# Kernel tuning notes

Measured on AMD Instinct MI355X. Metric: run time of the kernel, lower is better.

## Reference

```python
import jax, jax.numpy as jnp
import numpy as np

B, N, C, H = 4, 2048, 1024, 16
D = C // H  # head_dim = 64

def setup_inputs() -> dict:
    key = jax.random.key(0)
    k1, k2, k3, k4, k5, k6 = jax.random.split(key, 6)
    x = jax.random.normal(k1, (B, N, C), dtype=jnp.float32)
    rope_cos = jax.random.uniform(k2, (N, D), dtype=jnp.float32)
    rope_sin = jax.random.uniform(k3, (N, D), dtype=jnp.float32)
    w_qkv = jax.random.normal(k4, (3 * C, C), dtype=jnp.float32) * (C ** -0.5)
    w_proj = jax.random.normal(k5, (C, C), dtype=jnp.float32) * (C ** -0.5)
    b_proj = jax.random.normal(k6, (C,), dtype=jnp.float32) * 0.01
    return {"x": x, "rope_cos": rope_cos, "rope_sin": rope_sin,
            "w_qkv": w_qkv, "w_proj": w_proj, "b_proj": b_proj}

def _rotate_half(x):
    x1, x2 = jnp.split(x, 2, axis=-1)
    return jnp.concatenate((-x2, x1), axis=-1)

def _apply_rope(x, cos, sin):
    # x: [B,H,N,D]; cos/sin: [N,D] broadcast over B,H
    return x * cos + _rotate_half(x) * sin

def reference(x, rope_cos, rope_sin, w_qkv, w_proj, b_proj):
    Bc, Nc, Cc = x.shape
    scale = D ** -0.5
    qkv = jnp.einsum('bnc,fc->bnf', x, w_qkv)            # [B,N,3C]
    qkv = qkv.reshape(Bc, Nc, 3, H, D).transpose(2, 0, 3, 1, 4)  # [3,B,H,N,D]
    q, k, v = qkv[0], qkv[1], qkv[2]
    q = _apply_rope(q, rope_cos, rope_sin)
    k = _apply_rope(k, rope_cos, rope_sin)
    attn = jnp.einsum('bhnd,bhmd->bhnm', q, k) * scale   # [B,H,N,N]
    attn = jax.nn.softmax(attn, axis=-1)
    out = jnp.einsum('bhnm,bhmd->bhnd', attn, v)         # [B,H,N,D]
    out = out.transpose(0, 2, 1, 3).reshape(Bc, Nc, Cc)  # [B,N,C]
    return jnp.einsum('bnc,fc->bnf', out, w_proj) + b_proj
```

## Files before the change

kernel.cpp:

```cpp
#include <hip/hip_runtime.h>

#define MM   8192
#define CC   1024
#define F3   3072
#define NN   2048
#define HH   16
#define DD   64
#define QSCALE 0.1803368801111731f

typedef __attribute__((ext_vector_type(8))) __bf16 bf16x8;
typedef __attribute__((ext_vector_type(4))) float floatx4;
typedef __attribute__((ext_vector_type(4))) unsigned uintx4;

__device__ __forceinline__ unsigned short f2b(float f) {
  union { float f; unsigned int u; } v; v.f = f;
  unsigned int r = v.u + 0x7fffu + ((v.u >> 16) & 1u);
  return (unsigned short)(r >> 16);
}
__device__ __forceinline__ float b2f(unsigned short b) {
  union { unsigned int u; float f; } v; v.u = ((unsigned int)b) << 16;
  return v.f;
}

__device__ __forceinline__ void gl_lds16(const unsigned short* g, unsigned short* l) {
  __builtin_amdgcn_global_load_lds((const __attribute__((address_space(1))) void*)g,
                                   (__attribute__((address_space(3))) void*)l, 16, 0, 0);
}

__global__ __launch_bounds__(256) void f32_to_bf16_k(const float* __restrict__ in,
                                                     unsigned short* __restrict__ out, int n4) {
  int i = blockIdx.x * 256 + threadIdx.x;
  if (i < n4) {
    float4 v = ((const float4*)in)[i];
    ushort4 o;
    o.x = f2b(v.x); o.y = f2b(v.y); o.z = f2b(v.z); o.w = f2b(v.w);
    ((ushort4*)out)[i] = o;
  }
}

template <int F, bool BF16OUT, bool ROPE>
__global__ __launch_bounds__(256) void gemm_bt(const unsigned short* __restrict__ A,
                                               const unsigned short* __restrict__ Bm,
                                               void* __restrict__ Cout,
                                               const float* __restrict__ bias,
                                               const float* __restrict__ rcp,
                                               const float* __restrict__ spp, int K) {
  __shared__ alignas(16) unsigned short lA[128 * 32];
  __shared__ alignas(16) unsigned short lB[128 * 32];
  const int tid = threadIdx.x, lane = tid & 63, wave = tid >> 6;
  const int r16 = lane & 15, q4 = lane >> 4;
  const int rowBase = blockIdx.x * 128, colBase = blockIdx.y * 128;
  const int wm = wave & 1, wf = wave >> 1;

  floatx4 acc[4][4];
  const floatx4 z = {0.f, 0.f, 0.f, 0.f};
  for (int i = 0; i < 4; ++i)
    for (int j = 0; j < 4; ++j) acc[i][j] = z;

  for (int k0 = 0; k0 < K; k0 += 32) {
    __syncthreads();
#pragma unroll
    for (int i = 0; i < 2; ++i) {
      int chunk = i * 256 + tid;
      int row = chunk >> 2, col = (chunk & 3) * 8;
      gl_lds16(A + (size_t)(rowBase + row) * K + k0 + col, &lA[chunk * 8]);
      gl_lds16(Bm + (size_t)(colBase + row) * K + k0 + col, &lB[chunk * 8]);
    }
    __syncthreads();
    bf16x8 af[4];
    for (int im = 0; im < 4; ++im)
      af[im] = *(const bf16x8*)(&lA[(wm * 64 + im * 16 + r16) * 32 + q4 * 8]);
    for (int jf = 0; jf < 4; ++jf) {
      bf16x8 bfr = *(const bf16x8*)(&lB[(wf * 64 + jf * 16 + r16) * 32 + q4 * 8]);
      for (int im = 0; im < 4; ++im)
        acc[im][jf] = __builtin_amdgcn_mfma_f32_16x16x32_bf16(af[im], bfr, acc[im][jf], 0, 0, 0);
    }
  }

  if (ROPE) {
    int head = (colBase >> 6) + wf;
    if (head < 32) {
      const bool isq = head < 16;
      for (int im = 0; im < 4; ++im)
        for (int jf = 0; jf < 2; ++jf)
          for (int r = 0; r < 4; ++r) {
            int grow = rowBase + wm * 64 + im * 16 + q4 * 4 + r;
            int n = grow & (NN - 1);
            int dp = jf * 16 + r16;
            float x0 = acc[im][jf][r], x1 = acc[im][jf + 2][r];
            float c0 = rcp[n * DD + dp],      s0v = spp[n * DD + dp];
            float c1 = rcp[n * DD + dp + 32], s1v = spp[n * DD + dp + 32];
            float y0 = x0 * c0 - x1 * s0v;
            float y1 = x1 * c1 + x0 * s1v;
            if (isq) { y0 *= QSCALE; y1 *= QSCALE; }
            acc[im][jf][r] = y0;
            acc[im][jf + 2][r] = y1;
          }
    }
  }

  for (int im = 0; im < 4; ++im)
    for (int jf = 0; jf < 4; ++jf)
      for (int r = 0; r < 4; ++r) {
        int grow = rowBase + wm * 64 + im * 16 + q4 * 4 + r;
        int gcol = colBase + wf * 64 + jf * 16 + r16;
        if (BF16OUT)
          ((unsigned short*)Cout)[(size_t)grow * F + gcol] = f2b(acc[im][jf][r]);
        else
          ((float*)Cout)[(size_t)grow * F + gcol] = acc[im][jf][r] + bias[gcol];
      }
}

__global__ __launch_bounds__(256, 4) void attn_k(const unsigned short* __restrict__ qkv,
                                                 unsigned short* __restrict__ obuf) {
  __shared__ alignas(16) unsigned short sK[64 * 64];
  __shared__ alignas(16) unsigned short sVT[64 * 64];

  const int tid = threadIdx.x, lane = tid & 63, wave = tid >> 6;
  const int r16 = lane & 15, q4 = lane >> 4;

  const int id = blockIdx.x + (int)gridDim.x * blockIdx.y;
  const int xcd = id & 7, slot = id >> 3;
  const int bh = xcd * 8 + (slot >> 4);
  const int q0 = (slot & 15) * 128;
  const int b = bh >> 4, h = bh & 15;
  const unsigned short* qbase = qkv + (size_t)(b * NN) * F3 + h * DD;

  bf16x8 qf[2][2];
#pragma unroll
  for (int im = 0; im < 2; ++im)
#pragma unroll
    for (int kk = 0; kk < 2; ++kk)
      qf[im][kk] = *(const bf16x8*)(qbase +
          (size_t)(q0 + wave * 32 + im * 16 + r16) * F3 + kk * 32 + q4 * 8);

  const floatx4 z = {0.f, 0.f, 0.f, 0.f};
  floatx4 o[2][4];
  float lacc[2] = {0.f, 0.f};
#pragma unroll
  for (int im = 0; im < 2; ++im)
    for (int jd = 0; jd < 4; ++jd) o[im][jd] = z;

  const int krow0 = tid >> 3, kc8 = tid & 7;
  const int vkvp = tid >> 3, vc8 = tid & 7;
  const int mp = (vkvp & 16) | ((vkvp & 4) << 1) | ((vkvp & 2) << 1) |
                 ((vkvp & 8) >> 2) | (vkvp & 1);

  const unsigned short* kvb = qbase;
  int4 kreg0 = *(const int4*)(kvb + (size_t)krow0 * F3 + CC + kc8 * 8);
  int4 kreg1 = *(const int4*)(kvb + (size_t)(krow0 + 32) * F3 + CC + kc8 * 8);
  int4 vreg0 = *(const int4*)(kvb + (size_t)(2 * vkvp) * F3 + 2 * CC + vc8 * 8);
  int4 vreg1 = *(const int4*)(kvb + (size_t)(2 * vkvp + 1) * F3 + 2 * CC + vc8 * 8);

  for (int t = 0; t < NN / 64; ++t) {
    __syncthreads();

    *(int4*)(&sK[krow0 * 64 + ((kc8 ^ (krow0 & 7)) << 3)]) = kreg0;
    *(int4*)(&sK[(krow0 + 32) * 64 + ((kc8 ^ ((krow0 + 32) & 7)) << 3)]) = kreg1;
    {
      const unsigned* a0 = (const unsigned*)&vreg0;
      const unsigned* a1 = (const unsigned*)&vreg1;
#pragma unroll
      for (int w = 0; w < 4; ++w) {
        unsigned lo = __builtin_amdgcn_perm(a1[w], a0[w], 0x05040100u);
        unsigned hi = __builtin_amdgcn_perm(a1[w], a0[w], 0x07060302u);
        int d0 = vc8 * 8 + 2 * w;
        int sw0 = (2 * w + vc8) & 7;
        int sw1 = (2 * w + 1 + vc8) & 7;
        *(unsigned*)(&sVT[d0 * 64 + (((mp >> 2) ^ sw0) << 3) + 2 * (mp & 3)]) = lo;
        *(unsigned*)(&sVT[(d0 + 1) * 64 + (((mp >> 2) ^ sw1) << 3) + 2 * (mp & 3)]) = hi;
      }
    }

    if (t + 1 < NN / 64) {
      const unsigned short* nb = qkv + (size_t)(b * NN + (t + 1) * 64) * F3 + h * DD;
      kreg0 = *(const int4*)(nb + (size_t)krow0 * F3 + CC + kc8 * 8);
      kreg1 = *(const int4*)(nb + (size_t)(krow0 + 32) * F3 + CC + kc8 * 8);
      vreg0 = *(const int4*)(nb + (size_t)(2 * vkvp) * F3 + 2 * CC + vc8 * 8);
      vreg1 = *(const int4*)(nb + (size_t)(2 * vkvp + 1) * F3 + 2 * CC + vc8 * 8);
    }

    __syncthreads();

    floatx4 s[2][4];
    __builtin_amdgcn_s_setprio(1);
#pragma unroll
    for (int jn = 0; jn < 4; ++jn) {
      int row = jn * 16 + r16;
      bf16x8 kf0 = *(const bf16x8*)(&sK[row * 64 + ((q4 ^ (row & 7)) << 3)]);
      bf16x8 kf1 = *(const bf16x8*)(&sK[row * 64 + (((4 + q4) ^ (row & 7)) << 3)]);
#pragma unroll
      for (int im = 0; im < 2; ++im) {
        floatx4 a = z;
        a = __builtin_amdgcn_mfma_f32_16x16x32_bf16(kf0, qf[im][0], a, 0, 0, 0);
        a = __builtin_amdgcn_mfma_f32_16x16x32_bf16(kf1, qf[im][1], a, 0, 0, 0);
        s[im][jn] = a;
      }
    }
    __builtin_amdgcn_s_setprio(0);

    bf16x8 pf[2][2];
#pragma unroll
    for (int im = 0; im < 2; ++im) {
#pragma unroll
      for (int kk = 0; kk < 2; ++kk) {
        uintx4 pk;
#pragma unroll
        for (int j2 = 0; j2 < 2; ++j2) {
          int jn = 2 * kk + j2;
          float p0 = __builtin_amdgcn_exp2f(s[im][jn][0]);
          float p1 = __builtin_amdgcn_exp2f(s[im][jn][1]);
          float p2 = __builtin_amdgcn_exp2f(s[im][jn][2]);
          float p3 = __builtin_amdgcn_exp2f(s[im][jn][3]);
          lacc[im] += (p0 + p1) + (p2 + p3);
          asm("v_cvt_pk_bf16_f32 %0, %1, %2" : "=v"(pk[2 * j2]) : "v"(p0), "v"(p1));
          asm("v_cvt_pk_bf16_f32 %0, %1, %2" : "=v"(pk[2 * j2 + 1]) : "v"(p2), "v"(p3));
        }
        pf[im][kk] = __builtin_bit_cast(bf16x8, pk);
      }
    }

    __builtin_amdgcn_s_setprio(1);
#pragma unroll
    for (int jd = 0; jd < 4; ++jd) {
      int d = jd * 16 + r16;
      int swr = (d + (d >> 3)) & 7;
      bf16x8 vf0 = *(const bf16x8*)(&sVT[d * 64 + ((q4 ^ swr) << 3)]);
      bf16x8 vf1 = *(const bf16x8*)(&sVT[d * 64 + (((4 + q4) ^ swr) << 3)]);
#pragma unroll
      for (int im = 0; im < 2; ++im) {
        o[im][jd] = __builtin_amdgcn_mfma_f32_16x16x32_bf16(pf[im][0], vf0, o[im][jd], 0, 0, 0);
        o[im][jd] = __builtin_amdgcn_mfma_f32_16x16x32_bf16(pf[im][1], vf1, o[im][jd], 0, 0, 0);
      }
    }
    __builtin_amdgcn_s_setprio(0);
  }

#pragma unroll
  for (int im = 0; im < 2; ++im) {
    float l = lacc[im];
    l += __shfl_xor(l, 16);
    l += __shfl_xor(l, 32);
    float inv = 1.0f / l;
#pragma unroll
    for (int r = 0; r < 4; ++r) {
      float invr = __shfl(inv, q4 * 4 + r);
      int row = q0 + wave * 32 + im * 16 + q4 * 4 + r;
#pragma unroll
      for (int jd = 0; jd < 4; ++jd) {
        int col = h * DD + jd * 16 + r16;
        obuf[(size_t)(b * NN + row) * CC + col] = f2b(o[im][jd][r] * invr);
      }
    }
  }
}

extern "C" void kernel_launch(void* const* d_in, const int* in_sizes, int n_in,
                              void* d_out, int out_size, void* d_ws, size_t ws_size,
                              hipStream_t stream) {
  const float* x     = (const float*)d_in[0];
  const float* rc    = (const float*)d_in[1];
  const float* rs    = (const float*)d_in[2];
  const float* wqkv  = (const float*)d_in[3];
  const float* wproj = (const float*)d_in[4];
  const float* bproj = (const float*)d_in[5];
  float* out = (float*)d_out;

  char* w = (char*)d_ws;
  unsigned short* xb     = (unsigned short*)(w);
  unsigned short* wqkvb  = (unsigned short*)(w + 16777216);
  unsigned short* wprojb = (unsigned short*)(w + 23068672);
  unsigned short* qkvb   = (unsigned short*)(w + 25165824);
  unsigned short* obuf   = (unsigned short*)(w + 75497472);

  f32_to_bf16_k<<<(MM * CC / 4 + 255) / 256, 256, 0, stream>>>(x, xb, MM * CC / 4);
  f32_to_bf16_k<<<(F3 * CC / 4 + 255) / 256, 256, 0, stream>>>(wqkv, wqkvb, F3 * CC / 4);
  f32_to_bf16_k<<<(CC * CC / 4 + 255) / 256, 256, 0, stream>>>(wproj, wprojb, CC * CC / 4);

  gemm_bt<F3, true, true><<<dim3(MM / 128, F3 / 128), 256, 0, stream>>>(
      xb, wqkvb, qkvb, nullptr, rc, rs, CC);

  attn_k<<<dim3(NN / 128, 4 * HH), 256, 0, stream>>>(qkvb, obuf);

  gemm_bt<CC, false, false><<<dim3(MM / 128, CC / 128), 256, 0, stream>>>(
      obuf, wprojb, out, bproj, nullptr, nullptr, CC);
}
```

Baseline: 286.7 us.

## Rewrite GEMMs with triple-buffered LDS pipeline, XOR swizzle, and XCD-aware tiling

Replaces the single-buffered 128x128 GEMM with a 512-thread 128x256 tile kernel. It prefetches three 64-wide K stages into LDS through direct global-to-LDS loads, stores them with an XOR swizzle to avoid bank conflicts, and maps blocks across XCDs for L2 locality. The aim is to hide global load latency and cut the barrier count per K step for both the QKV and projection GEMMs. The cost is much larger LDS use (about 144KB per block), which limits occupancy. The 1D launch grid also assumes fixed problem dimensions.

```diff
diff --git a/kernel.cpp b/kernel.cpp
--- a/kernel.cpp
+++ b/kernel.cpp
@@ -39,50 +39,106 @@
 }
 
 template <int F, bool BF16OUT, bool ROPE>
-__global__ __launch_bounds__(256) void gemm_bt(const unsigned short* __restrict__ A,
-                                               const unsigned short* __restrict__ Bm,
-                                               void* __restrict__ Cout,
-                                               const float* __restrict__ bias,
-                                               const float* __restrict__ rcp,
-                                               const float* __restrict__ spp, int K) {
-  __shared__ alignas(16) unsigned short lA[128 * 32];
-  __shared__ alignas(16) unsigned short lB[128 * 32];
+__global__ __launch_bounds__(512, 2) void gemm_p(const unsigned short* __restrict__ A,
+                                                 const unsigned short* __restrict__ Bm,
+                                                 void* __restrict__ Cout,
+                                                 const float* __restrict__ bias,
+                                                 const float* __restrict__ rcp,
+                                                 const float* __restrict__ spp, int K) {
+  __shared__ alignas(16) unsigned short lA[3][128 * 64];
+  __shared__ alignas(16) unsigned short lB[3][256 * 64];
   const int tid = threadIdx.x, lane = tid & 63, wave = tid >> 6;
   const int r16 = lane & 15, q4 = lane >> 4;
-  const int rowBase = blockIdx.x * 128, colBase = blockIdx.y * 128;
-  const int wm = wave & 1, wf = wave >> 1;
+  const int wm = wave & 1, wn = wave >> 1;
+
+  const int id = blockIdx.x;
+  const int xcd = id & 7, slot = id >> 3;
+  const int rx = xcd * 8 + (slot & 7), cy = slot >> 3;
+  const int rowBase = rx * 128, colBase = cy * 256;
+
+  const int cA0 = tid, cA1 = tid + 512;
+  const int cB0 = tid, cB1 = tid + 512, cB2 = tid + 1024, cB3 = tid + 1536;
+#define CHOFF(base, c) ((size_t)((base) + ((c) >> 3)) * K + ((((c) & 7) ^ (((c) >> 3) & 7)) << 3))
+  const size_t aoff0 = CHOFF(rowBase, cA0), aoff1 = CHOFF(rowBase, cA1);
+  const size_t boff0 = CHOFF(colBase, cB0), boff1 = CHOFF(colBase, cB1);
+  const size_t boff2 = CHOFF(colBase, cB2), boff3 = CHOFF(colBase, cB3);
+#undef CHOFF
+
+#define STAGEP(kt, bsel) do { const int _k0 = (kt) * 64; \
+    gl_lds16(A + aoff0 + _k0, &lA[bsel][cA0 * 8]); \
+    gl_lds16(A + aoff1 + _k0, &lA[bsel][cA1 * 8]); \
+    gl_lds16(Bm + boff0 + _k0, &lB[bsel][cB0 * 8]); \
+    gl_lds16(Bm + boff1 + _k0, &lB[bsel][cB1 * 8]); \
+    gl_lds16(Bm + boff2 + _k0, &lB[bsel][cB2 * 8]); \
+    gl_lds16(Bm + boff3 + _k0, &lB[bsel][cB3 * 8]); } while (0)
 
   floatx4 acc[4][4];
   const floatx4 z = {0.f, 0.f, 0.f, 0.f};
+#pragma unroll
   for (int i = 0; i < 4; ++i)
+#pragma unroll
     for (int j = 0; j < 4; ++j) acc[i][j] = z;
 
-  for (int k0 = 0; k0 < K; k0 += 32) {
-    __syncthreads();
-#pragma unroll
-    for (int i = 0; i < 2; ++i) {
-      int chunk = i * 256 + tid;
-      int row = chunk >> 2, col = (chunk & 3) * 8;
-      gl_lds16(A + (size_t)(rowBase + row) * K + k0 + col, &lA[chunk * 8]);
-      gl_lds16(Bm + (size_t)(colBase + row) * K + k0 + col, &lB[chunk * 8]);
-    }
-    __syncthreads();
-    bf16x8 af[4];
-    for (int im = 0; im < 4; ++im)
-      af[im] = *(const bf16x8*)(&lA[(wm * 64 + im * 16 + r16) * 32 + q4 * 8]);
+  const int nt = K / 64;
+
+  STAGEP(0, 0);
+  STAGEP(1, 1);
+  STAGEP(2, 2);
+  asm volatile("s_waitcnt vmcnt(12)" ::: "memory");
+  __builtin_amdgcn_s_barrier();
+  __builtin_amdgcn_sched_barrier(0);
+
+  int bs = 0;
+  for (int t = 0; t < nt; ++t) {
+    const unsigned short* la = &lA[bs][0];
+    const unsigned short* lb = &lB[bs][0];
+    bf16x8 af[4][2], bv[4][2];
+#pragma unroll
+    for (int im = 0; im < 4; ++im) {
+      int row = wm * 64 + im * 16 + r16, r7 = row & 7;
+      af[im][0] = *(const bf16x8*)(la + row * 64 + ((q4 ^ r7) << 3));
+      af[im][1] = *(const bf16x8*)(la + row * 64 + (((4 + q4) ^ r7) << 3));
+    }
+#pragma unroll
     for (int jf = 0; jf < 4; ++jf) {
-      bf16x8 bfr = *(const bf16x8*)(&lB[(wf * 64 + jf * 16 + r16) * 32 + q4 * 8]);
-      for (int im = 0; im < 4; ++im)
-        acc[im][jf] = __builtin_amdgcn_mfma_f32_16x16x32_bf16(af[im], bfr, acc[im][jf], 0, 0, 0);
-    }
-  }
+      int row = wn * 64 + jf * 16 + r16, r7 = row & 7;
+      bv[jf][0] = *(const bf16x8*)(lb + row * 64 + ((q4 ^ r7) << 3));
+      bv[jf][1] = *(const bf16x8*)(lb + row * 64 + (((4 + q4) ^ r7) << 3));
+    }
+    __builtin_amdgcn_s_setprio(1);
+#pragma unroll
+    for (int jf = 0; jf < 4; ++jf)
+#pragma unroll
+      for (int im = 0; im < 4; ++im) {
+        acc[im][jf] = __builtin_amdgcn_mfma_f32_16x16x32_bf16(af[im][0], bv[jf][0], acc[im][jf], 0, 0, 0);
+        acc[im][jf] = __builtin_amdgcn_mfma_f32_16x16x32_bf16(af[im][1], bv[jf][1], acc[im][jf], 0, 0, 0);
+      }
+    __builtin_amdgcn_s_setprio(0);
+
+    __builtin_amdgcn_s_barrier();
+    __builtin_amdgcn_sched_barrier(0);
+    if (t + 3 < nt) {
+      STAGEP(t + 3, bs);
+      asm volatile("s_waitcnt vmcnt(12)" ::: "memory");
+    } else {
+      asm volatile("s_waitcnt vmcnt(0)" ::: "memory");
+    }
+    __builtin_amdgcn_sched_barrier(0);
+    __builtin_amdgcn_s_barrier();
+    __builtin_amdgcn_sched_barrier(0);
+    bs = (bs == 2) ? 0 : bs + 1;
+  }
+#undef STAGEP
 
   if (ROPE) {
-    int head = (colBase >> 6) + wf;
+    int head = (colBase >> 6) + wn;
     if (head < 32) {
       const bool isq = head < 16;
+#pragma unroll
       for (int im = 0; im < 4; ++im)
+#pragma unroll
         for (int jf = 0; jf < 2; ++jf)
+#pragma unroll
           for (int r = 0; r < 4; ++r) {
             int grow = rowBase + wm * 64 + im * 16 + q4 * 4 + r;
             int n = grow & (NN - 1);
@@ -99,11 +155,14 @@
     }
   }
 
+#pragma unroll
   for (int im = 0; im < 4; ++im)
+#pragma unroll
     for (int jf = 0; jf < 4; ++jf)
+#pragma unroll
       for (int r = 0; r < 4; ++r) {
         int grow = rowBase + wm * 64 + im * 16 + q4 * 4 + r;
-        int gcol = colBase + wf * 64 + jf * 16 + r16;
+        int gcol = colBase + wn * 64 + jf * 16 + r16;
         if (BF16OUT)
           ((unsigned short*)Cout)[(size_t)grow * F + gcol] = f2b(acc[im][jf][r]);
         else
@@ -277,11 +336,11 @@
   f32_to_bf16_k<<<(F3 * CC / 4 + 255) / 256, 256, 0, stream>>>(wqkv, wqkvb, F3 * CC / 4);
   f32_to_bf16_k<<<(CC * CC / 4 + 255) / 256, 256, 0, stream>>>(wproj, wprojb, CC * CC / 4);
 
-  gemm_bt<F3, true, true><<<dim3(MM / 128, F3 / 128), 256, 0, stream>>>(
+  gemm_p<F3, true, true><<<768, 512, 0, stream>>>(
       xb, wqkvb, qkvb, nullptr, rc, rs, CC);
 
   attn_k<<<dim3(NN / 128, 4 * HH), 256, 0, stream>>>(qkvb, obuf);
 
-  gemm_bt<CC, false, false><<<dim3(MM / 128, CC / 128), 256, 0, stream>>>(
+  gemm_p<CC, false, false><<<256, 512, 0, stream>>>(
       obuf, wprojb, out, bproj, nullptr, nullptr, CC);
 }
```

Measured after the change: 279.2 us. -2.6%, faster.
